# Kernel optimization log

Hardware: AMD Instinct MI355X
Metric: run time of the kernel (lower is better)

Reference implementation:

```python
import jax, jax.numpy as jnp
import numpy as np


def setup_inputs() -> dict:
    key = jax.random.key(0)
    ks = jax.random.split(key, 8)
    B, C, H, W = 4, 64, 64, 64
    s = 1.0 / np.sqrt(C)
    return {
        "x": jax.random.normal(ks[0], (B, C, H, W), jnp.float32),
        "W1": jax.random.normal(ks[1], (C, C), jnp.float32) * s,
        "b1": jax.random.normal(ks[2], (C,), jnp.float32) * 0.01,
        "W2": jax.random.normal(ks[3], (C, C), jnp.float32) * s,
        "b2": jax.random.normal(ks[4], (C,), jnp.float32) * 0.01,
        "W3": jax.random.normal(ks[5], (C, C), jnp.float32) * s,
        "b3": jax.random.normal(ks[6], (C,), jnp.float32) * 0.01,
        "alpha": jax.random.normal(ks[7], (1,), jnp.float32) * 0.1,
    }


def reference(x, W1, b1, W2, b2, W3, b3, alpha):
    B, C, H, W = x.shape
    N = H * W
    xf = x.reshape(B, C, N)  # flatten spatial dims
    # 1x1 convs == per-pixel linear maps over channels
    q = jnp.einsum('oc,bcn->bno', W1, xf) + b1                 # (B, N, C)
    k = jnp.einsum('oc,bcn->bon', W2, xf) + b2[None, :, None]  # (B, C, N)
    v = jnp.einsum('oc,bcn->bon', W3, xf) + b3[None, :, None]  # (B, C, N)
    # full spatial attention, no scaling (matches original)
    S = jax.nn.softmax(jnp.einsum('bnc,bcm->bnm', q, k), axis=-1)  # (B, N, N)
    # E = D @ S^T : out pixel n aggregates values at m with weight S[n, m]
    E = jnp.einsum('bcm,bnm->bcn', v, S)
    return x + alpha[0] * E.reshape(B, C, H, W)
```

## Files before the change

kernel.cpp:

```cpp
#include <hip/hip_runtime.h>

typedef __attribute__((ext_vector_type(8)))  short          short8;
typedef __attribute__((ext_vector_type(16))) float          f32x16;
typedef __attribute__((ext_vector_type(8)))  unsigned short ushort8;
typedef __attribute__((ext_vector_type(4)))  unsigned int   uint4v;

#define B_    4
#define C_    64
#define N_    4096
#define LOG2E 1.4426950408889634f

__device__ __forceinline__ unsigned short f2bf(float f) {
    unsigned u = __builtin_bit_cast(unsigned, f);
    return (unsigned short)((u + 0x7FFFu + ((u >> 16) & 1u)) >> 16);
}
__device__ __forceinline__ float bf2f(unsigned short h) {
    return __builtin_bit_cast(float, (unsigned)h << 16);
}
__device__ __forceinline__ float fexp2(float x) {
    float r; asm("v_exp_f32 %0, %1" : "=v"(r) : "v"(x)); return r;
}
__device__ __forceinline__ unsigned pkbf(float lo, float hi) {
    unsigned r; asm("v_cvt_pk_bf16_f32 %0, %1, %2" : "=v"(r) : "v"(lo), "v"(hi));
    return r;
}
__device__ __forceinline__ f32x16 mfma32(short8 a, short8 b, f32x16 c) {
    return __builtin_amdgcn_mfma_f32_32x32x16_bf16(a, b, c, 0, 0, 0);
}

__global__ __launch_bounds__(256) void qkv_proj(
    const float* __restrict__ x,
    const float* __restrict__ W1, const float* __restrict__ b1,
    const float* __restrict__ W2, const float* __restrict__ b2,
    const float* __restrict__ W3, const float* __restrict__ b3,
    unsigned short* __restrict__ qh_g, unsigned short* __restrict__ ql_g,
    unsigned short* __restrict__ kh_g, unsigned short* __restrict__ kl_g,
    unsigned short* __restrict__ v_g)
{
    __shared__ unsigned short Vl[64][72];

    const int tid = threadIdx.x;
    const int tn  = tid & 63;
    const int to  = __builtin_amdgcn_readfirstlane(tid >> 6);
    const int b   = blockIdx.y;
    const int n0  = blockIdx.x * 64;
    const int n   = n0 + tn;

    const float* xb = x + (size_t)b * C_ * N_;
    float xv[64];
    #pragma unroll
    for (int c = 0; c < 64; ++c) xv[c] = xb[c * N_ + n];

    ushort8 qh8[2], ql8[2], kh8[2], kl8[2];
    #pragma unroll
    for (int og = 0; og < 16; ++og) {
        const int o = to * 16 + og;
        const float4* w1r = (const float4*)(W1 + o * 64);
        const float4* w2r = (const float4*)(W2 + o * 64);
        const float4* w3r = (const float4*)(W3 + o * 64);
        float aq = b1[o], ak = b2[o], av = b3[o];
        #pragma unroll
        for (int c4 = 0; c4 < 16; ++c4) {
            float4 w1v = w1r[c4], w2v = w2r[c4], w3v = w3r[c4];
            const float x0 = xv[4*c4+0], x1 = xv[4*c4+1], x2 = xv[4*c4+2], x3 = xv[4*c4+3];
            aq = fmaf(w1v.x, x0, aq); aq = fmaf(w1v.y, x1, aq);
            aq = fmaf(w1v.z, x2, aq); aq = fmaf(w1v.w, x3, aq);
            ak = fmaf(w2v.x, x0, ak); ak = fmaf(w2v.y, x1, ak);
            ak = fmaf(w2v.z, x2, ak); ak = fmaf(w2v.w, x3, ak);
            av = fmaf(w3v.x, x0, av); av = fmaf(w3v.y, x1, av);
            av = fmaf(w3v.z, x2, av); av = fmaf(w3v.w, x3, av);
        }
        ak *= LOG2E;
        const int s = og >> 3, e = og & 7;
        unsigned short hsh;
        hsh = f2bf(aq); qh8[s][e] = hsh; ql8[s][e] = f2bf(aq - bf2f(hsh));
        hsh = f2bf(ak); kh8[s][e] = hsh; kl8[s][e] = f2bf(ak - bf2f(hsh));
        Vl[o][tn] = f2bf(av);
    }

    const size_t base = (size_t)b * N_ * 64;
    const int blk = ((n >> 5) * 4 + to) * 512;
    #pragma unroll
    for (int hh = 0; hh < 2; ++hh) {
        const int off = blk + (hh * 32 + (n & 31)) * 8;
        *(ushort8*)(qh_g + base + off) = qh8[hh];
        *(ushort8*)(ql_g + base + off) = ql8[hh];
        *(ushort8*)(kh_g + base + off) = kh8[hh];
        *(ushort8*)(kl_g + base + off) = kl8[hh];
    }
    __syncthreads();

    #pragma unroll
    for (int i = 0; i < 2; ++i) {
        const int chunk = tid + 256 * i;
        const int lane = chunk & 63;
        const int ct   = (chunk >> 6) & 1;
        const int ksl  = chunk >> 7;
        const int c    = ct * 32 + (lane & 31);
        const int nl   = ksl * 16 + (lane >> 5) * 8;
        ushort8 vv = *(const ushort8*)&Vl[c][nl];
        *(ushort8*)(v_g + base + (size_t)((((n0 >> 4) + ksl) * 2 + ct) * 512) + lane * 8) = vv;
    }
}

__global__ __launch_bounds__(512) void flash_attn(
    const unsigned short* __restrict__ qh_g, const unsigned short* __restrict__ ql_g,
    const unsigned short* __restrict__ kh_g, const unsigned short* __restrict__ kl_g,
    const unsigned short* __restrict__ v_g,
    const float* __restrict__ x, const float* __restrict__ alpha_p,
    float* __restrict__ out)
{
    __shared__ float Part[4][64][32];
    __shared__ float Ml[4][2][32];

    const int tid  = threadIdx.x;
    const int l    = tid & 63;
    const int w    = __builtin_amdgcn_readfirstlane(tid >> 6);
    const int h    = l >> 5;
    const int qcol = l & 31;
    const int qsub = w & 1;
    const int ksl  = w >> 1;

    const int bid = blockIdx.x;
    const int b   = (bid & 7) >> 1;
    const int qt  = ((bid >> 3) << 1) | (bid & 1);
    const int q0  = qt * 64;

    const size_t base = (size_t)b * N_ * 64;
    const unsigned short* qhB = qh_g + base;
    const unsigned short* qlB = ql_g + base;
    const unsigned short* khB = kh_g + base;
    const unsigned short* klB = kl_g + base;
    const unsigned short* vB  = v_g  + base;

    const int qblk = (q0 >> 5) + qsub;
    short8 qh[4], ql[4];
    #pragma unroll
    for (int ds = 0; ds < 4; ++ds) {
        qh[ds] = *(const short8*)(qhB + (qblk * 4 + ds) * 512 + l * 8);
        ql[ds] = *(const short8*)(qlB + (qblk * 4 + ds) * 512 + l * 8);
    }

    f32x16 o0, o1;
    #pragma unroll
    for (int r = 0; r < 16; ++r) { o0[r] = 0.f; o1[r] = 0.f; }
    float m = -1e30f, lsum = 0.f;

    #pragma unroll 1
    for (int tt = 0; tt < 32; ++tt) {
        const int kb = ksl * 32 + tt;

        short8 kh[4], klo[4];
        #pragma unroll
        for (int ds = 0; ds < 4; ++ds) {
            kh[ds]  = *(const short8*)(khB + (kb * 4 + ds) * 512 + l * 8);
            klo[ds] = *(const short8*)(klB + (kb * 4 + ds) * 512 + l * 8);
        }
        short8 vfr[2][2];
        #pragma unroll
        for (int sp = 0; sp < 2; ++sp)
            #pragma unroll
            for (int ct = 0; ct < 2; ++ct)
                vfr[sp][ct] = *(const short8*)(vB + (size_t)(((kb * 2 + sp) * 2 + ct) * 512) + l * 8);

        f32x16 a0, a1, a2;
        #pragma unroll
        for (int r = 0; r < 16; ++r) { a0[r] = 0.f; a1[r] = 0.f; a2[r] = 0.f; }
        #pragma unroll
        for (int ds = 0; ds < 4; ++ds) a0 = mfma32(kh[ds],  qh[ds], a0);
        #pragma unroll
        for (int ds = 0; ds < 4; ++ds) a1 = mfma32(kh[ds],  ql[ds], a1);
        #pragma unroll
        for (int ds = 0; ds < 4; ++ds) a2 = mfma32(klo[ds], qh[ds], a2);
        f32x16 s = a0 + a1;
        s = s + a2;

        float t0 = fmaxf(s[0], s[1]),   t1 = fmaxf(s[2], s[3]);
        float t2 = fmaxf(s[4], s[5]),   t3 = fmaxf(s[6], s[7]);
        float t4 = fmaxf(s[8], s[9]),   t5 = fmaxf(s[10], s[11]);
        float t6 = fmaxf(s[12], s[13]), t7 = fmaxf(s[14], s[15]);
        t0 = fmaxf(t0, t1); t2 = fmaxf(t2, t3); t4 = fmaxf(t4, t5); t6 = fmaxf(t6, t7);
        float tm = fmaxf(fmaxf(t0, t2), fmaxf(t4, t6));
        tm = fmaxf(tm, __shfl_xor(tm, 32));
        const int need = (tm > m + 8.0f);
        if (__any(need)) {
            const float mn   = fmaxf(m, tm);
            const float corr = fexp2(m - mn);
            m = mn; lsum *= corr;
            o0 *= corr; o1 *= corr;
        }
        float p[16];
        #pragma unroll
        for (int r = 0; r < 16; ++r) p[r] = fexp2(s[r] - m);
        float ss = 0.f;
        #pragma unroll
        for (int r = 0; r < 16; ++r) ss += p[r];
        ss += __shfl_xor(ss, 32);
        lsum += ss;

        unsigned pw[4][2];
        #pragma unroll
        for (int mi = 0; mi < 4; ++mi) {
            pw[mi][0] = pkbf(p[4*mi+0], p[4*mi+1]);
            pw[mi][1] = pkbf(p[4*mi+2], p[4*mi+3]);
        }
        #pragma unroll
        for (int sp = 0; sp < 2; ++sp) {
            const unsigned send0 = h ? pw[2*sp][0] : pw[2*sp+1][0];
            const unsigned send1 = h ? pw[2*sp][1] : pw[2*sp+1][1];
            const unsigned r0 = (unsigned)__shfl_xor((int)send0, 32);
            const unsigned r1 = (unsigned)__shfl_xor((int)send1, 32);
            uint4v pi;
            pi[0] = h ? r0 : pw[2*sp][0];
            pi[1] = h ? r1 : pw[2*sp][1];
            pi[2] = h ? pw[2*sp+1][0] : r0;
            pi[3] = h ? pw[2*sp+1][1] : r1;
            const short8 pf = __builtin_bit_cast(short8, pi);
            o0 = mfma32(vfr[sp][0], pf, o0);
            o1 = mfma32(vfr[sp][1], pf, o1);
        }
    }

    const float alpha = alpha_p[0];
    #pragma unroll
    for (int rnd = 0; rnd < 2; ++rnd) {
        __syncthreads();
        if (qsub == rnd) {
            #pragma unroll
            for (int r = 0; r < 16; ++r) {
                const int crow = (r & 3) + 8 * (r >> 2) + 4 * h;
                Part[ksl][crow][qcol]      = o0[r];
                Part[ksl][32 + crow][qcol] = o1[r];
            }
            if (h == 0) { Ml[ksl][0][qcol] = m; Ml[ksl][1][qcol] = lsum; }
        }
        __syncthreads();
        const int q  = tid & 31;
        const int cg = tid >> 5;
        const float m0 = Ml[0][0][q], m1 = Ml[1][0][q], m2 = Ml[2][0][q], m3 = Ml[3][0][q];
        const float M  = fmaxf(fmaxf(m0, m1), fmaxf(m2, m3));
        const float w0 = fexp2(m0 - M), w1 = fexp2(m1 - M);
        const float w2 = fexp2(m2 - M), w3 = fexp2(m3 - M);
        const float L  = w0 * Ml[0][1][q] + w1 * Ml[1][1][q]
                       + w2 * Ml[2][1][q] + w3 * Ml[3][1][q];
        const float invL = 1.0f / L;
        #pragma unroll
        for (int j = 0; j < 4; ++j) {
            const int c = cg * 4 + j;
            const float e = w0 * Part[0][c][q] + w1 * Part[1][c][q]
                          + w2 * Part[2][c][q] + w3 * Part[3][c][q];
            const size_t idx = (size_t)(b * 64 + c) * N_ + q0 + rnd * 32 + q;
            out[idx] = x[idx] + alpha * e * invL;
        }
    }
}

extern "C" void kernel_launch(void* const* d_in, const int* in_sizes, int n_in,
                              void* d_out, int out_size, void* d_ws, size_t ws_size,
                              hipStream_t stream)
{
    const float* x     = (const float*)d_in[0];
    const float* W1    = (const float*)d_in[1];
    const float* b1    = (const float*)d_in[2];
    const float* W2    = (const float*)d_in[3];
    const float* b2    = (const float*)d_in[4];
    const float* W3    = (const float*)d_in[5];
    const float* b3    = (const float*)d_in[6];
    const float* alpha = (const float*)d_in[7];
    float* out = (float*)d_out;

    const size_t TEN = (size_t)B_ * N_ * C_;
    unsigned short* qh = (unsigned short*)d_ws;
    unsigned short* ql = qh + TEN;
    unsigned short* kh = ql + TEN;
    unsigned short* kl = kh + TEN;
    unsigned short* v  = kl + TEN;

    qkv_proj<<<dim3(N_ / 64, B_), 256, 0, stream>>>(x, W1, b1, W2, b2, W3, b3,
                                                    qh, ql, kh, kl, v);
    flash_attn<<<256, 512, 0, stream>>>(qh, ql, kh, kl, v, x, alpha, out);
}
```

Before: 160.4 us.

## Double-buffer K tile loads in flash attention and stage projection weights in LDS

The attention loop now prefetches the next K hi/lo tile into a second register buffer while the current tile is processed, unrolled by two, so global-load latency overlaps the MFMA and softmax work. Two of the three score accumulators are merged into one chain, and the kernel is given a waves-per-EU hint of 2. The projection kernel copies W1–W3 into shared memory once per block instead of reading them from global memory inside the inner loop. The extra buffers raise register pressure, which can cost occupancy or cause spills, and the 48 KB of weight LDS may limit how many projection blocks fit per CU.

```diff
diff --git a/kernel.cpp b/kernel.cpp
--- a/kernel.cpp
+++ b/kernel.cpp
@@ -23,6 +23,12 @@
 __device__ __forceinline__ unsigned pkbf(float lo, float hi) {
     unsigned r; asm("v_cvt_pk_bf16_f32 %0, %1, %2" : "=v"(r) : "v"(lo), "v"(hi));
     return r;
+}
+__device__ __forceinline__ float xhalf_max(float v) {
+    return fmaxf(v, __shfl_xor(v, 32));
+}
+__device__ __forceinline__ float xhalf_sum(float v) {
+    return v + __shfl_xor(v, 32);
 }
 __device__ __forceinline__ f32x16 mfma32(short8 a, short8 b, f32x16 c) {
     return __builtin_amdgcn_mfma_f32_32x32x16_bf16(a, b, c, 0, 0, 0);
@@ -37,6 +43,7 @@
     unsigned short* __restrict__ kh_g, unsigned short* __restrict__ kl_g,
     unsigned short* __restrict__ v_g)
 {
+    __shared__ __align__(16) float Wlds[3][64][64];
     __shared__ unsigned short Vl[64][72];
 
     const int tid = threadIdx.x;
@@ -46,22 +53,33 @@
     const int n0  = blockIdx.x * 64;
     const int n   = n0 + tn;
 
+    {
+        const float* Ws[3] = {W1, W2, W3};
+        #pragma unroll
+        for (int mtx = 0; mtx < 3; ++mtx)
+            #pragma unroll
+            for (int j = 0; j < 4; ++j) {
+                const int idx = j * 256 + tid;
+                ((float4*)&Wlds[mtx][0][0])[idx] = ((const float4*)Ws[mtx])[idx];
+            }
+    }
+
     const float* xb = x + (size_t)b * C_ * N_;
     float xv[64];
     #pragma unroll
     for (int c = 0; c < 64; ++c) xv[c] = xb[c * N_ + n];
+    __syncthreads();
 
     ushort8 qh8[2], ql8[2], kh8[2], kl8[2];
     #pragma unroll
     for (int og = 0; og < 16; ++og) {
         const int o = to * 16 + og;
-        const float4* w1r = (const float4*)(W1 + o * 64);
-        const float4* w2r = (const float4*)(W2 + o * 64);
-        const float4* w3r = (const float4*)(W3 + o * 64);
         float aq = b1[o], ak = b2[o], av = b3[o];
         #pragma unroll
         for (int c4 = 0; c4 < 16; ++c4) {
-            float4 w1v = w1r[c4], w2v = w2r[c4], w3v = w3r[c4];
+            const float4 w1v = *(const float4*)&Wlds[0][o][c4 * 4];
+            const float4 w2v = *(const float4*)&Wlds[1][o][c4 * 4];
+            const float4 w3v = *(const float4*)&Wlds[2][o][c4 * 4];
             const float x0 = xv[4*c4+0], x1 = xv[4*c4+1], x2 = xv[4*c4+2], x3 = xv[4*c4+3];
             aq = fmaf(w1v.x, x0, aq); aq = fmaf(w1v.y, x1, aq);
             aq = fmaf(w1v.z, x2, aq); aq = fmaf(w1v.w, x3, aq);
@@ -103,7 +121,8 @@
     }
 }
 
-__global__ __launch_bounds__(512) void flash_attn(
+__global__ __launch_bounds__(512) __attribute__((amdgpu_waves_per_eu(2)))
+void flash_attn(
     const unsigned short* __restrict__ qh_g, const unsigned short* __restrict__ ql_g,
     const unsigned short* __restrict__ kh_g, const unsigned short* __restrict__ kl_g,
     const unsigned short* __restrict__ v_g,
@@ -129,9 +148,9 @@
     const size_t base = (size_t)b * N_ * 64;
     const unsigned short* qhB = qh_g + base;
     const unsigned short* qlB = ql_g + base;
-    const unsigned short* khB = kh_g + base;
-    const unsigned short* klB = kl_g + base;
-    const unsigned short* vB  = v_g  + base;
+    const unsigned short* khG = kh_g + base;
+    const unsigned short* klG = kl_g + base;
+    const unsigned short* vG  = v_g  + base;
 
     const int qblk = (q0 >> 5) + qsub;
     short8 qh[4], ql[4];
@@ -146,80 +165,91 @@
     for (int r = 0; r < 16; ++r) { o0[r] = 0.f; o1[r] = 0.f; }
     float m = -1e30f, lsum = 0.f;
 
+    short8 khA[4], klA[4], khBuf[4], klBuf[4];
+
+#define LOADK(kb, KH, KL)                                                      \
+    {   const int _kb = (kb);                                                  \
+        _Pragma("unroll")                                                      \
+        for (int ds = 0; ds < 4; ++ds) {                                       \
+            KH[ds] = *(const short8*)(khG + (_kb * 4 + ds) * 512 + l * 8);     \
+            KL[ds] = *(const short8*)(klG + (_kb * 4 + ds) * 512 + l * 8);     \
+        }                                                                      \
+    }
+
+#define COMPUTE(kb, KH, KL)                                                    \
+    {   const int _kb = (kb);                                                  \
+        short8 vfr[2][2];                                                      \
+        _Pragma("unroll")                                                      \
+        for (int sp = 0; sp < 2; ++sp)                                         \
+            _Pragma("unroll")                                                  \
+            for (int ct = 0; ct < 2; ++ct)                                     \
+                vfr[sp][ct] = *(const short8*)(vG +                            \
+                    (size_t)(((_kb * 2 + sp) * 2 + ct) * 512) + l * 8);        \
+        f32x16 a0, a1;                                                         \
+        _Pragma("unroll")                                                      \
+        for (int r = 0; r < 16; ++r) { a0[r] = 0.f; a1[r] = 0.f; }             \
+        _Pragma("unroll")                                                      \
+        for (int ds = 0; ds < 4; ++ds) a0 = mfma32(KH[ds], qh[ds], a0);        \
+        _Pragma("unroll")                                                      \
+        for (int ds = 0; ds < 4; ++ds) a0 = mfma32(KL[ds], qh[ds], a0);        \
+        _Pragma("unroll")                                                      \
+        for (int ds = 0; ds < 4; ++ds) a1 = mfma32(KH[ds], ql[ds], a1);        \
+        f32x16 s = a0 + a1;                                                    \
+        float t0 = fmaxf(s[0], s[1]),   t1 = fmaxf(s[2], s[3]);                \
+        float t2 = fmaxf(s[4], s[5]),   t3 = fmaxf(s[6], s[7]);                \
+        float t4 = fmaxf(s[8], s[9]),   t5 = fmaxf(s[10], s[11]);              \
+        float t6 = fmaxf(s[12], s[13]), t7 = fmaxf(s[14], s[15]);              \
+        t0 = fmaxf(t0, t1); t2 = fmaxf(t2, t3);                                \
+        t4 = fmaxf(t4, t5); t6 = fmaxf(t6, t7);                                \
+        float tm = fmaxf(fmaxf(t0, t2), fmaxf(t4, t6));                        \
+        tm = xhalf_max(tm);                                                    \
+        const int need = (tm > m + 8.0f);                                      \
+        if (__any(need)) {                                                     \
+            const float mn   = fmaxf(m, tm);                                   \
+            const float corr = fexp2(m - mn);                                  \
+            m = mn; lsum *= corr;                                              \
+            o0 *= corr; o1 *= corr;                                            \
+        }                                                                      \
+        float p[16];                                                           \
+        _Pragma("unroll")                                                      \
+        for (int r = 0; r < 16; ++r) p[r] = fexp2(s[r] - m);                   \
+        float ss = 0.f;                                                        \
+        _Pragma("unroll")                                                      \
+        for (int r = 0; r < 16; ++r) ss += p[r];                               \
+        lsum += xhalf_sum(ss);                                                 \
+        unsigned pw[4][2];                                                     \
+        _Pragma("unroll")                                                      \
+        for (int mi = 0; mi < 4; ++mi) {                                       \
+            pw[mi][0] = pkbf(p[4*mi+0], p[4*mi+1]);                            \
+            pw[mi][1] = pkbf(p[4*mi+2], p[4*mi+3]);                            \
+        }                                                                      \
+        _Pragma("unroll")                                                      \
+        for (int sp = 0; sp < 2; ++sp) {                                       \
+            const unsigned send0 = h ? pw[2*sp][0] : pw[2*sp+1][0];            \
+            const unsigned send1 = h ? pw[2*sp][1] : pw[2*sp+1][1];            \
+            const unsigned r0 = (unsigned)__shfl_xor((int)send0, 32);          \
+            const unsigned r1 = (unsigned)__shfl_xor((int)send1, 32);          \
+            uint4v pi;                                                         \
+            pi[0] = h ? r0 : pw[2*sp][0];                                      \
+            pi[1] = h ? r1 : pw[2*sp][1];                                      \
+            pi[2] = h ? pw[2*sp+1][0] : r0;                                    \
+            pi[3] = h ? pw[2*sp+1][1] : r1;                                    \
+            const short8 pf = __builtin_bit_cast(short8, pi);                  \
+            o0 = mfma32(vfr[sp][0], pf, o0);                                   \
+            o1 = mfma32(vfr[sp][1], pf, o1);                                   \
+        }                                                                      \
+    }
+
+    LOADK(ksl * 32, khA, klA);
     #pragma unroll 1
-    for (int tt = 0; tt < 32; ++tt) {
-        const int kb = ksl * 32 + tt;
-
-        short8 kh[4], klo[4];
-        #pragma unroll
-        for (int ds = 0; ds < 4; ++ds) {
-            kh[ds]  = *(const short8*)(khB + (kb * 4 + ds) * 512 + l * 8);
-            klo[ds] = *(const short8*)(klB + (kb * 4 + ds) * 512 + l * 8);
-        }
-        short8 vfr[2][2];
-        #pragma unroll
-        for (int sp = 0; sp < 2; ++sp)
-            #pragma unroll
-            for (int ct = 0; ct < 2; ++ct)
-                vfr[sp][ct] = *(const short8*)(vB + (size_t)(((kb * 2 + sp) * 2 + ct) * 512) + l * 8);
-
-        f32x16 a0, a1, a2;
-        #pragma unroll
-        for (int r = 0; r < 16; ++r) { a0[r] = 0.f; a1[r] = 0.f; a2[r] = 0.f; }
-        #pragma unroll
-        for (int ds = 0; ds < 4; ++ds) a0 = mfma32(kh[ds],  qh[ds], a0);
-        #pragma unroll
-        for (int ds = 0; ds < 4; ++ds) a1 = mfma32(kh[ds],  ql[ds], a1);
-        #pragma unroll
-        for (int ds = 0; ds < 4; ++ds) a2 = mfma32(klo[ds], qh[ds], a2);
-        f32x16 s = a0 + a1;
-        s = s + a2;
-
-        float t0 = fmaxf(s[0], s[1]),   t1 = fmaxf(s[2], s[3]);
-        float t2 = fmaxf(s[4], s[5]),   t3 = fmaxf(s[6], s[7]);
-        float t4 = fmaxf(s[8], s[9]),   t5 = fmaxf(s[10], s[11]);
-        float t6 = fmaxf(s[12], s[13]), t7 = fmaxf(s[14], s[15]);
-        t0 = fmaxf(t0, t1); t2 = fmaxf(t2, t3); t4 = fmaxf(t4, t5); t6 = fmaxf(t6, t7);
-        float tm = fmaxf(fmaxf(t0, t2), fmaxf(t4, t6));
-        tm = fmaxf(tm, __shfl_xor(tm, 32));
-        const int need = (tm > m + 8.0f);
-        if (__any(need)) {
-            const float mn   = fmaxf(m, tm);
-            const float corr = fexp2(m - mn);
-            m = mn; lsum *= corr;
-            o0 *= corr; o1 *= corr;
-        }
-        float p[16];
-        #pragma unroll
-        for (int r = 0; r < 16; ++r) p[r] = fexp2(s[r] - m);
-        float ss = 0.f;
-        #pragma unroll
-        for (int r = 0; r < 16; ++r) ss += p[r];
-        ss += __shfl_xor(ss, 32);
-        lsum += ss;
-
-        unsigned pw[4][2];
-        #pragma unroll
-        for (int mi = 0; mi < 4; ++mi) {
-            pw[mi][0] = pkbf(p[4*mi+0], p[4*mi+1]);
-            pw[mi][1] = pkbf(p[4*mi+2], p[4*mi+3]);
-        }
-        #pragma unroll
-        for (int sp = 0; sp < 2; ++sp) {
-            const unsigned send0 = h ? pw[2*sp][0] : pw[2*sp+1][0];
-            const unsigned send1 = h ? pw[2*sp][1] : pw[2*sp+1][1];
-            const unsigned r0 = (unsigned)__shfl_xor((int)send0, 32);
-            const unsigned r1 = (unsigned)__shfl_xor((int)send1, 32);
-            uint4v pi;
-            pi[0] = h ? r0 : pw[2*sp][0];
-            pi[1] = h ? r1 : pw[2*sp][1];
-            pi[2] = h ? pw[2*sp+1][0] : r0;
-            pi[3] = h ? pw[2*sp+1][1] : r1;
-            const short8 pf = __builtin_bit_cast(short8, pi);
-            o0 = mfma32(vfr[sp][0], pf, o0);
-            o1 = mfma32(vfr[sp][1], pf, o1);
-        }
-    }
+    for (int tt = 0; tt < 32; tt += 2) {
+        LOADK(ksl * 32 + tt + 1, khBuf, klBuf);
+        COMPUTE(ksl * 32 + tt, khA, klA);
+        if (tt + 2 < 32) LOADK(ksl * 32 + tt + 2, khA, klA);
+        COMPUTE(ksl * 32 + tt + 1, khBuf, klBuf);
+    }
+#undef LOADK
+#undef COMPUTE
 
     const float alpha = alpha_p[0];
     #pragma unroll
```

Result: faster. 133.4 us (-16.9%).
